# Performance work log

Hardware: AMD Instinct MI355X
Metric: run time of the kernel (lower is better)

The kernel has to match this reference:

```python
import math
import jax, jax.numpy as jnp
import numpy as np

B, L, NS = 8, 1024, 512
D, NH, DN = 512, 8, 256
E, K, HE = 8, 2, 2048
EPS = 1e-5


def setup_inputs() -> dict:
    key = jax.random.key(0)
    ks = jax.random.split(key, 40)
    def rn(i, shape, s=0.02):
        return jax.random.normal(ks[i], shape, jnp.float32) * s
    inp = {
        'x': jax.random.normal(ks[0], (B, L, D), jnp.float32),
        'scene_tokens': jax.random.normal(ks[1], (B, NS, D), jnp.float32),
        't': jax.random.uniform(ks[2], (B,), jnp.float32) * 1000.0,
        # scene LayerNorm (affine)
        'scene_norm_g': jnp.ones((D,), jnp.float32),
        'scene_norm_b': jnp.zeros((D,), jnp.float32),
        # scene cross-attn projections (stored [in,out])
        'ca_wq': rn(3, (D, D)), 'ca_bq': jnp.zeros((D,)),
        'ca_wk': rn(4, (D, D)), 'ca_bk': jnp.zeros((D,)),
        'ca_wv': rn(5, (D, D)), 'ca_bv': jnp.zeros((D,)),
        'ca_wo': rn(6, (D, D)), 'ca_bo': jnp.zeros((D,)),
        # self-attn projections
        'sa_wq': rn(7, (D, D)), 'sa_bq': jnp.zeros((D,)),
        'sa_wk': rn(8, (D, D)), 'sa_bk': jnp.zeros((D,)),
        'sa_wv': rn(9, (D, D)), 'sa_bv': jnp.zeros((D,)),
        'sa_wo': rn(10, (D, D)), 'sa_bo': jnp.zeros((D,)),
        # noise_embed MLP: Linear(D,DN) -> SiLU -> Linear(DN,DN)
        'ne_w1': rn(11, (D, DN)), 'ne_b1': jnp.zeros((DN,)),
        'ne_w2': rn(12, (DN, DN)), 'ne_b2': jnp.zeros((DN,)),
        # AdaLN modulations: Linear(DN, 2D)
        'ncsa_mod_w': rn(13, (DN, 2 * D)), 'ncsa_mod_b': jnp.zeros((2 * D,)),
        'moe_mod_w': rn(14, (DN, 2 * D)), 'moe_mod_b': jnp.zeros((2 * D,)),
        # router
        'router_w': rn(15, (DN, E), s=0.1),
        # stacked pose-branch experts: fc_in D->2*HE, fc_out HE->D
        'fc_in_w': rn(16, (E, D, 2 * HE)), 'fc_in_b': jnp.zeros((E, 2 * HE)),
        'fc_out_w': rn(17, (E, HE, D)), 'fc_out_b': jnp.zeros((E, D)),
    }
    return inp


def _ln(x):
    mu = x.mean(-1, keepdims=True)
    var = ((x - mu) ** 2).mean(-1, keepdims=True)
    return (x - mu) * jax.lax.rsqrt(var + EPS)


def _mha(q_in, k_in, v_in, wq, bq, wk, bk, wv, bv, wo, bo):
    b, lq, d = q_in.shape
    lk = k_in.shape[1]
    hd = d // NH
    q = (q_in @ wq + bq).reshape(b, lq, NH, hd)
    k = (k_in @ wk + bk).reshape(b, lk, NH, hd)
    v = (v_in @ wv + bv).reshape(b, lk, NH, hd)
    att = jnp.einsum('bqhd,bkhd->bhqk', q, k) / math.sqrt(hd)
    p = jax.nn.softmax(att, axis=-1)
    o = jnp.einsum('bhqk,bkhd->bqhd', p, v).reshape(b, lq, d)
    return o @ wo + bo


def reference(x, scene_tokens, t,
              scene_norm_g, scene_norm_b,
              ca_wq, ca_bq, ca_wk, ca_bk, ca_wv, ca_bv, ca_wo, ca_bo,
              sa_wq, sa_bq, sa_wk, sa_bk, sa_wv, sa_bv, sa_wo, sa_bo,
              ne_w1, ne_b1, ne_w2, ne_b2,
              ncsa_mod_w, ncsa_mod_b, moe_mod_w, moe_mod_b,
              router_w, fc_in_w, fc_in_b, fc_out_w, fc_out_b):
    # --- noise clock embedding: sinusoidal(t, D) -> MLP ---
    half = D // 2
    freqs = jnp.exp(-math.log(10000.0) * jnp.arange(half, dtype=jnp.float32) / (half - 1))
    ang = t[:, None] * freqs[None, :]
    temb = jnp.concatenate([jnp.cos(ang), jnp.sin(ang)], axis=-1)  # [B, D]
    nc = jax.nn.silu(temb @ ne_w1 + ne_b1) @ ne_w2 + ne_b2  # [B, DN]

    # --- scene cross-attention ---
    x_in = _ln(x) * scene_norm_g + scene_norm_b
    x = x + _mha(x_in, scene_tokens, scene_tokens,
                 ca_wq, ca_bq, ca_wk, ca_bk, ca_wv, ca_bv, ca_wo, ca_bo)

    # --- noise-conditioned self-attention (AdaLN) ---
    mod = nc @ ncsa_mod_w + ncsa_mod_b
    shift, scale = jnp.split(mod, 2, axis=-1)
    x_ncsa = _ln(x) * (1.0 + scale[:, None, :]) + shift[:, None, :]
    x = x + _mha(x_ncsa, x_ncsa, x_ncsa,
                 sa_wq, sa_bq, sa_wk, sa_bk, sa_wv, sa_bv, sa_wo, sa_bo)

    # --- pose branch: AdaLN + noise-conditioned MoE ---
    mod = nc @ moe_mod_w + moe_mod_b
    shift, scale = jnp.split(mod, 2, axis=-1)
    x_moe = _ln(x) * (1.0 + scale[:, None, :]) + shift[:, None, :]

    logits = nc @ router_w  # temperature = 1.0
    probs = jax.nn.softmax(logits, axis=-1)
    tw, ti = jax.lax.top_k(probs, K)  # [B,K]
    tw = tw / jnp.clip(tw.sum(-1, keepdims=True), 1e-8)

    # gather per-sample selected expert weights -> grouped GEMM
    Wi = fc_in_w[ti]   # [B,K,D,2HE]
    bi = fc_in_b[ti]   # [B,K,2HE]
    h = jnp.einsum('bld,bkdh->bklh', x_moe, Wi) + bi[:, :, None, :]
    val, gate = jnp.split(h, 2, axis=-1)
    hid = val * jax.nn.silu(gate)   # [B,K,L,HE]
    Wo = fc_out_w[ti]  # [B,K,HE,D]
    bo = fc_out_b[ti]  # [B,K,D]
    eo = jnp.einsum('bklh,bkhd->bkld', hid, Wo) + bo[:, :, None, :]
    mixed = jnp.einsum('bk,bkld->bld', tw, eo)

    return x + mixed
```

## Files before the change

### kernel.cpp

```cpp
#include <hip/hip_runtime.h>
#include <math.h>

typedef unsigned short ushort_t;
typedef __attribute__((ext_vector_type(8))) short short8;
typedef __attribute__((ext_vector_type(4))) float f32x4;

#define B_   8
#define L_   1024
#define NS_  512
#define D_   512
#define NH_  8
#define HE_  2048
#define EPS_ 1e-5f

#define MFMA16(a, b, c) __builtin_amdgcn_mfma_f32_16x16x32_bf16(a, b, c, 0, 0, 0)
#define GL2LDS(g, l) __builtin_amdgcn_global_load_lds( \
    (const __attribute__((address_space(1))) unsigned int*)(g), \
    (__attribute__((address_space(3))) unsigned int*)(l), 16, 0, 0)

__device__ __forceinline__ ushort_t f2bf(float f) {
  unsigned u = __float_as_uint(f);
  unsigned r = (u + 0x7fffu + ((u >> 16) & 1u)) >> 16;
  return (ushort_t)r;
}

__device__ __forceinline__ void stage_tile(const ushort_t* __restrict__ g0,
                                           int ld, ushort_t* lds) {
  const int t = threadIdx.x;
  const int w = t >> 6, lane = t & 63;
#pragma unroll
  for (int j = 0; j < 2; ++j) {
    const int c = w * 64 + j * 256 + lane;
    const int row = c >> 2, col = (c & 3) * 8;
    GL2LDS(g0 + (size_t)row * ld + col, lds + (size_t)(w * 64 + j * 256) * 8);
  }
}

__global__ __launch_bounds__(256) void noise_embed(
    const float* __restrict__ t_in,
    const float* __restrict__ w1, const float* __restrict__ b1,
    const float* __restrict__ w2, const float* __restrict__ b2,
    const float* __restrict__ rw,
    float* __restrict__ nc_out,
    float* __restrict__ tw_out, int* __restrict__ ti_out)
{
  const int b = blockIdx.x;
  const int t = threadIdx.x;
  __shared__ float temb[512];
  __shared__ float h1[256];
  __shared__ float ncs[256];
  const float tv = t_in[b];
  {
    float fr = __expf(-logf(10000.0f) * (float)t / 255.0f);
    float ang = tv * fr;
    temb[t] = cosf(ang);
    temb[256 + t] = sinf(ang);
  }
  __syncthreads();
  {
    float s = b1[t];
#pragma unroll 8
    for (int i = 0; i < 512; ++i) s += temb[i] * w1[i * 256 + t];
    h1[t] = s / (1.0f + __expf(-s));
  }
  __syncthreads();
  {
    float s = b2[t];
#pragma unroll 8
    for (int i = 0; i < 256; ++i) s += h1[i] * w2[i * 256 + t];
    ncs[t] = s;
    nc_out[b * 256 + t] = s;
  }
  __syncthreads();
  if (t == 0) {
    float lg[8];
    for (int e = 0; e < 8; ++e) {
      float s = 0.f;
      for (int i = 0; i < 256; ++i) s += ncs[i] * rw[i * 8 + e];
      lg[e] = s;
    }
    float mx = lg[0];
    for (int e = 1; e < 8; ++e) mx = fmaxf(mx, lg[e]);
    float z = 0.f, p[8];
    for (int e = 0; e < 8; ++e) { p[e] = __expf(lg[e] - mx); z += p[e]; }
    for (int e = 0; e < 8; ++e) p[e] /= z;
    int i0 = 0;
    for (int e = 1; e < 8; ++e) if (p[e] > p[i0]) i0 = e;
    int i1 = (i0 == 0) ? 1 : 0;
    for (int e = 0; e < 8; ++e) if (e != i0 && p[e] > p[i1]) i1 = e;
    float s01 = fmaxf(p[i0] + p[i1], 1e-8f);
    tw_out[b * 2 + 0] = p[i0] / s01;
    tw_out[b * 2 + 1] = p[i1] / s01;
    ti_out[b * 2 + 0] = i0;
    ti_out[b * 2 + 1] = i1;
  }
}

__global__ __launch_bounds__(256) void mod_proj(
    const float* __restrict__ nc,
    const float* __restrict__ ncsa_w, const float* __restrict__ ncsa_b,
    const float* __restrict__ moe_w, const float* __restrict__ moe_b,
    float* __restrict__ ncsa_mod, float* __restrict__ moe_mod)
{
  const int b = blockIdx.x, cg = blockIdx.y;
  const int t = threadIdx.x;
  __shared__ float ncs[256];
  ncs[t] = nc[b * 256 + t];
  __syncthreads();
  const int col = cg * 128 + (t & 127);
  const int half = t >> 7;
  const float* wsel = half ? moe_w : ncsa_w;
  const float* bsel = half ? moe_b : ncsa_b;
  float* osel = half ? moe_mod : ncsa_mod;
  float s = bsel[col];
#pragma unroll 8
  for (int i = 0; i < 256; ++i) s += ncs[i] * wsel[(size_t)i * 1024 + col];
  osel[b * 1024 + col] = s;
}

__global__ __launch_bounds__(256) void ln_mod_kernel(
    const float* __restrict__ X, const float* __restrict__ gvec,
    const float* __restrict__ bvec, const float* __restrict__ mod,
    ushort_t* __restrict__ Y)
{
  const int row = blockIdx.x;
  const int b = row >> 10;
  const int t = threadIdx.x;
  const float* xr = X + (size_t)row * 512;
  float2 v = *(const float2*)(xr + t * 2);
  float s = v.x + v.y;
  float q = v.x * v.x + v.y * v.y;
#pragma unroll
  for (int off = 32; off > 0; off >>= 1) {
    s += __shfl_down(s, off, 64);
    q += __shfl_down(q, off, 64);
  }
  __shared__ float ws_[4], wq_[4], smu[1], sinv[1];
  if ((t & 63) == 0) { ws_[t >> 6] = s; wq_[t >> 6] = q; }
  __syncthreads();
  if (t == 0) {
    float S = ws_[0] + ws_[1] + ws_[2] + ws_[3];
    float Q = wq_[0] + wq_[1] + wq_[2] + wq_[3];
    float mu = S * (1.0f / 512.0f);
    float var = Q * (1.0f / 512.0f) - mu * mu;
    smu[0] = mu;
    sinv[0] = rsqrtf(var + EPS_);
  }
  __syncthreads();
  const float mu = smu[0], inv = sinv[0];
  const int d0 = t * 2;
  float scx, scy, shx, shy;
  if (mod) {
    const float* mrow = mod + (size_t)b * 1024;
    scx = 1.0f + mrow[512 + d0]; scy = 1.0f + mrow[512 + d0 + 1];
    shx = mrow[d0];              shy = mrow[d0 + 1];
  } else {
    scx = gvec[d0]; scy = gvec[d0 + 1];
    shx = bvec[d0]; shy = bvec[d0 + 1];
  }
  float ox = (v.x - mu) * inv * scx + shx;
  float oy = (v.y - mu) * inv * scy + shy;
  unsigned pk = (unsigned)f2bf(ox) | ((unsigned)f2bf(oy) << 16);
  *(unsigned*)(Y + (size_t)row * 512 + d0) = pk;
}

__global__ __launch_bounds__(256) void transpose_cvt(
    const float* __restrict__ in, ushort_t* __restrict__ out,
    int R, int C, long ibs, long obs)
{
  __shared__ float tile[32][33];
  const float* src = in + (size_t)blockIdx.z * ibs;
  ushort_t* dst = out + (size_t)blockIdx.z * obs;
  const int c0 = blockIdx.x * 32, r0 = blockIdx.y * 32;
  const int tx = threadIdx.x & 31, ty = threadIdx.x >> 5;
  for (int rr = ty; rr < 32; rr += 8)
    tile[rr][tx] = src[(size_t)(r0 + rr) * C + c0 + tx];
  __syncthreads();
  for (int rr = ty; rr < 32; rr += 8)
    dst[(size_t)(c0 + rr) * R + r0 + tx] = f2bf(tile[tx][rr]);
}

struct P8 { const float* p[8]; };
__global__ __launch_bounds__(256) void transpose_cvt8(
    P8 srcs, ushort_t* __restrict__ out)
{
  __shared__ float tile[32][33];
  const float* src = srcs.p[blockIdx.z];
  ushort_t* dst = out + (size_t)blockIdx.z * 512 * 512;
  const int c0 = blockIdx.x * 32, r0 = blockIdx.y * 32;
  const int tx = threadIdx.x & 31, ty = threadIdx.x >> 5;
  for (int rr = ty; rr < 32; rr += 8)
    tile[rr][tx] = src[(size_t)(r0 + rr) * 512 + c0 + tx];
  __syncthreads();
  for (int rr = ty; rr < 32; rr += 8)
    dst[(size_t)(c0 + rr) * 512 + r0 + tx] = f2bf(tile[tx][rr]);
}

__global__ __launch_bounds__(256) void cvt_bf16(
    const float* __restrict__ in, ushort_t* __restrict__ out)
{
  const int i = (blockIdx.x * 256 + threadIdx.x) * 4;
  float4 v = *(const float4*)(in + i);
  uint2 pk;
  pk.x = (unsigned)f2bf(v.x) | ((unsigned)f2bf(v.y) << 16);
  pk.y = (unsigned)f2bf(v.z) | ((unsigned)f2bf(v.w) << 16);
  *(uint2*)(out + i) = pk;
}

__global__ __launch_bounds__(256) void gemm_bf16(
    const ushort_t* __restrict__ A, const ushort_t* __restrict__ Bt,
    const float* __restrict__ bias, const float* __restrict__ resid,
    void* __restrict__ Cout, int M, int N, int K, int bf16_out)
{
  __shared__ ushort_t As[2][4096];
  __shared__ ushort_t Bs[2][4096];
  const int t = threadIdx.x;
  const int w = t >> 6, lane = t & 63;
  const int quad = lane >> 4, r = lane & 15;
  const int wm = w >> 1, wn = w & 1;
  const int bm = blockIdx.y * 128, bn = blockIdx.x * 128;
  f32x4 acc[4][4];
#pragma unroll
  for (int i = 0; i < 4; ++i)
#pragma unroll
    for (int j = 0; j < 4; ++j) acc[i][j] = (f32x4){0.f, 0.f, 0.f, 0.f};
  const ushort_t* Ab = A + (size_t)bm * K;
  const ushort_t* Bb = Bt + (size_t)bn * K;
  const int NIT = K >> 5;
  stage_tile(Ab, K, As[0]);
  stage_tile(Bb, K, Bs[0]);
  __syncthreads();
  for (int it = 0; it < NIT; ++it) {
    const int cur = it & 1;
    if (it + 1 < NIT) {
      stage_tile(Ab + (it + 1) * 32, K, As[cur ^ 1]);
      stage_tile(Bb + (it + 1) * 32, K, Bs[cur ^ 1]);
    }
    short8 af[4], bfg[4];
#pragma unroll
    for (int i = 0; i < 4; ++i)
      af[i] = *(const short8*)&As[cur][(wm * 64 + i * 16 + r) * 32 + quad * 8];
#pragma unroll
    for (int j = 0; j < 4; ++j)
      bfg[j] = *(const short8*)&Bs[cur][(wn * 64 + j * 16 + r) * 32 + quad * 8];
#pragma unroll
    for (int i = 0; i < 4; ++i)
#pragma unroll
      for (int j = 0; j < 4; ++j)
        acc[i][j] = MFMA16(af[i], bfg[j], acc[i][j]);
    __syncthreads();
  }
  if (bf16_out) {
    ushort_t* Cb = (ushort_t*)Cout;
#pragma unroll
    for (int j = 0; j < 4; ++j) {
      const int col = bn + wn * 64 + j * 16 + r;
      const float bia = bias[col];
#pragma unroll
      for (int i = 0; i < 4; ++i)
#pragma unroll
        for (int reg = 0; reg < 4; ++reg) {
          const int row = bm + wm * 64 + i * 16 + quad * 4 + reg;
          Cb[(size_t)row * N + col] = f2bf(acc[i][j][reg] + bia);
        }
    }
  } else {
    float* Cf = (float*)Cout;
#pragma unroll
    for (int j = 0; j < 4; ++j) {
      const int col = bn + wn * 64 + j * 16 + r;
      const float bia = bias[col];
#pragma unroll
      for (int i = 0; i < 4; ++i)
#pragma unroll
        for (int reg = 0; reg < 4; ++reg) {
          const int row = bm + wm * 64 + i * 16 + quad * 4 + reg;
          float v = acc[i][j][reg] + bia;
          if (resid) v += resid[(size_t)row * N + col];
          Cf[(size_t)row * N + col] = v;
        }
    }
  }
}

__global__ __launch_bounds__(256, 2) void fattn_mfma(
    const ushort_t* __restrict__ Q, const ushort_t* __restrict__ Kmat,
    const ushort_t* __restrict__ V, ushort_t* __restrict__ O, int Lk)
{
  __shared__ __align__(16) ushort_t Ks[64][72];
  __shared__ __align__(16) ushort_t Vt[64][72];
  __shared__ __align__(16) ushort_t Pt[4][32][72];
  const int t = threadIdx.x;
  const int w = t >> 6, lane = t & 63;
  const int quad = lane >> 4, r = lane & 15;
  const int h = blockIdx.y, b = blockIdx.z;
  const int q0 = blockIdx.x * 128;
  const size_t hoff = (size_t)h * 64;
  const ushort_t* Qb = Q + ((size_t)b * 1024 + q0) * 512 + hoff;
  const ushort_t* Kb = Kmat + (size_t)b * Lk * 512 + hoff;
  const ushort_t* Vb = V + (size_t)b * Lk * 512 + hoff;

  short8 qb[2][2];
#pragma unroll
  for (int ct = 0; ct < 2; ++ct)
#pragma unroll
    for (int ki = 0; ki < 2; ++ki)
      qb[ct][ki] = *(const short8*)(Qb + (size_t)(w * 32 + ct * 16 + r) * 512 +
                                    ki * 32 + quad * 8);

  f32x4 oacc[4][2];
#pragma unroll
  for (int rt = 0; rt < 4; ++rt)
#pragma unroll
    for (int ct = 0; ct < 2; ++ct) oacc[rt][ct] = (f32x4){0.f, 0.f, 0.f, 0.f};
  float m_[2] = {-1e30f, -1e30f};
  float l_[2] = {0.f, 0.f};

  uint4 kr[2], vr[2], kn[2], vn[2];
  auto ldkv = [&](int k0, uint4* kp, uint4* vp) {
#pragma unroll
    for (int j = 0; j < 2; ++j) {
      const int dof = (w + 4 * j) * 8;
      kp[j] = *(const uint4*)(Kb + (size_t)(k0 + lane) * 512 + dof);
      vp[j] = *(const uint4*)(Vb + (size_t)(k0 + lane) * 512 + dof);
    }
  };
  auto stkv = [&](const uint4* kp, const uint4* vp) {
#pragma unroll
    for (int j = 0; j < 2; ++j) {
      const int dof = (w + 4 * j) * 8;
      *(uint4*)&Ks[lane][dof] = kp[j];
      const ushort_t* vv = (const ushort_t*)&vp[j];
#pragma unroll
      for (int i = 0; i < 8; ++i) Vt[dof + i][lane] = vv[i];
    }
  };

  ldkv(0, kr, vr);
  const int nch = Lk >> 6;
  for (int c = 0; c < nch; ++c) {
    stkv(kr, vr);
    __syncthreads();
    if (c + 1 < nch) ldkv((c + 1) << 6, kn, vn);

    f32x4 sacc[4][2];
#pragma unroll
    for (int rt = 0; rt < 4; ++rt)
#pragma unroll
      for (int ct = 0; ct < 2; ++ct) sacc[rt][ct] = (f32x4){0.f, 0.f, 0.f, 0.f};
#pragma unroll
    for (int ki = 0; ki < 2; ++ki) {
      short8 kf[4];
#pragma unroll
      for (int rt = 0; rt < 4; ++rt)
        kf[rt] = *(const short8*)&Ks[rt * 16 + r][ki * 32 + quad * 8];
#pragma unroll
      for (int rt = 0; rt < 4; ++rt)
#pragma unroll
        for (int ct = 0; ct < 2; ++ct)
          sacc[rt][ct] = MFMA16(kf[rt], qb[ct][ki], sacc[rt][ct]);
    }

#pragma unroll
    for (int ct = 0; ct < 2; ++ct) {
      float vmax = sacc[0][ct][0];
#pragma unroll
      for (int rt = 0; rt < 4; ++rt)
#pragma unroll
        for (int reg = 0; reg < 4; ++reg) vmax = fmaxf(vmax, sacc[rt][ct][reg]);
      vmax = fmaxf(vmax, __shfl_xor(vmax, 16, 64));
      vmax = fmaxf(vmax, __shfl_xor(vmax, 32, 64));
      const float mnew = fmaxf(m_[ct], vmax * 0.125f);
      const float corr = __expf(m_[ct] - mnew);
      m_[ct] = mnew;
      float ps = 0.f;
#pragma unroll
      for (int rt = 0; rt < 4; ++rt) {
        float p0 = __expf(fmaf(sacc[rt][ct][0], 0.125f, -mnew));
        float p1 = __expf(fmaf(sacc[rt][ct][1], 0.125f, -mnew));
        float p2 = __expf(fmaf(sacc[rt][ct][2], 0.125f, -mnew));
        float p3 = __expf(fmaf(sacc[rt][ct][3], 0.125f, -mnew));
        ps += (p0 + p1) + (p2 + p3);
        uint2 pk;
        pk.x = (unsigned)f2bf(p0) | ((unsigned)f2bf(p1) << 16);
        pk.y = (unsigned)f2bf(p2) | ((unsigned)f2bf(p3) << 16);
        *(uint2*)&Pt[w][ct * 16 + r][rt * 16 + quad * 4] = pk;
      }
      ps += __shfl_xor(ps, 16, 64);
      ps += __shfl_xor(ps, 32, 64);
      l_[ct] = l_[ct] * corr + ps;
#pragma unroll
      for (int rt = 0; rt < 4; ++rt)
#pragma unroll
        for (int reg = 0; reg < 4; ++reg) oacc[rt][ct][reg] *= corr;
    }

#pragma unroll
    for (int ki = 0; ki < 2; ++ki) {
      short8 vf[4], pf[2];
#pragma unroll
      for (int rt = 0; rt < 4; ++rt)
        vf[rt] = *(const short8*)&Vt[rt * 16 + r][ki * 32 + quad * 8];
#pragma unroll
      for (int ct = 0; ct < 2; ++ct)
        pf[ct] = *(const short8*)&Pt[w][ct * 16 + r][ki * 32 + quad * 8];
#pragma unroll
      for (int rt = 0; rt < 4; ++rt)
#pragma unroll
        for (int ct = 0; ct < 2; ++ct)
          oacc[rt][ct] = MFMA16(vf[rt], pf[ct], oacc[rt][ct]);
    }
    __syncthreads();
#pragma unroll
    for (int j = 0; j < 2; ++j) { kr[j] = kn[j]; vr[j] = vn[j]; }
  }

#pragma unroll
  for (int ct = 0; ct < 2; ++ct) {
    const float inv = 1.0f / l_[ct];
    const int qg = q0 + w * 32 + ct * 16 + r;
    ushort_t* op = O + ((size_t)b * 1024 + qg) * 512 + hoff;
#pragma unroll
    for (int rt = 0; rt < 4; ++rt) {
      uint2 pk;
      pk.x = (unsigned)f2bf(oacc[rt][ct][0] * inv) |
             ((unsigned)f2bf(oacc[rt][ct][1] * inv) << 16);
      pk.y = (unsigned)f2bf(oacc[rt][ct][2] * inv) |
             ((unsigned)f2bf(oacc[rt][ct][3] * inv) << 16);
      *(uint2*)(op + rt * 16 + quad * 4) = pk;
    }
  }
}

__global__ __launch_bounds__(256) void moe_fcin(
    const ushort_t* __restrict__ Xm, const ushort_t* __restrict__ WiT,
    const float* __restrict__ Bi, const float* __restrict__ tw,
    const int* __restrict__ ti, ushort_t* __restrict__ Hid, int ks)
{
  __shared__ ushort_t As[2][4096];
  __shared__ ushort_t Bv[2][4096];
  __shared__ ushort_t Bg[2][4096];
  const int t = threadIdx.x;
  const int w = t >> 6, lane = t & 63;
  const int quad = lane >> 4, r = lane & 15;
  const int wm = w >> 1, wn = w & 1;
  const int b = blockIdx.z;
  const int e = ti[b * 2 + ks];
  const float wq = tw[b * 2 + ks];
  const int r0 = blockIdx.y * 128, n0 = blockIdx.x * 128;
  const ushort_t* Ab = Xm + ((size_t)b * 1024 + r0) * 512;
  const ushort_t* Wv = WiT + (size_t)e * 4096 * 512 + (size_t)n0 * 512;
  const ushort_t* Wg = Wv + (size_t)2048 * 512;
  f32x4 av[4][4], ag[4][4];
#pragma unroll
  for (int i = 0; i < 4; ++i)
#pragma unroll
    for (int j = 0; j < 4; ++j) {
      av[i][j] = (f32x4){0.f, 0.f, 0.f, 0.f};
      ag[i][j] = (f32x4){0.f, 0.f, 0.f, 0.f};
    }
  stage_tile(Ab, 512, As[0]);
  stage_tile(Wv, 512, Bv[0]);
  stage_tile(Wg, 512, Bg[0]);
  __syncthreads();
  for (int it = 0; it < 16; ++it) {
    const int cur = it & 1;
    if (it + 1 < 16) {
      stage_tile(Ab + (it + 1) * 32, 512, As[cur ^ 1]);
      stage_tile(Wv + (it + 1) * 32, 512, Bv[cur ^ 1]);
      stage_tile(Wg + (it + 1) * 32, 512, Bg[cur ^ 1]);
    }
    short8 af[4], bv[4], bg[4];
#pragma unroll
    for (int i = 0; i < 4; ++i)
      af[i] = *(const short8*)&As[cur][(wm * 64 + i * 16 + r) * 32 + quad * 8];
#pragma unroll
    for (int j = 0; j < 4; ++j) {
      bv[j] = *(const short8*)&Bv[cur][(wn * 64 + j * 16 + r) * 32 + quad * 8];
      bg[j] = *(const short8*)&Bg[cur][(wn * 64 + j * 16 + r) * 32 + quad * 8];
    }
#pragma unroll
    for (int i = 0; i < 4; ++i)
#pragma unroll
      for (int j = 0; j < 4; ++j) {
        av[i][j] = MFMA16(af[i], bv[j], av[i][j]);
        ag[i][j] = MFMA16(af[i], bg[j], ag[i][j]);
      }
    __syncthreads();
  }
  ushort_t* Hb = Hid + (size_t)b * 1024 * 2048;
#pragma unroll
  for (int j = 0; j < 4; ++j) {
    const int col = n0 + wn * 64 + j * 16 + r;
    const float bval = Bi[(size_t)e * 4096 + col];
    const float bgat = Bi[(size_t)e * 4096 + 2048 + col];
#pragma unroll
    for (int i = 0; i < 4; ++i)
#pragma unroll
      for (int reg = 0; reg < 4; ++reg) {
        const int lrow = r0 + wm * 64 + i * 16 + quad * 4 + reg;
        float vv = av[i][j][reg] + bval;
        float gg = ag[i][j][reg] + bgat;
        float hv = vv * (gg / (1.0f + __expf(-gg))) * wq;
        Hb[(size_t)lrow * 2048 + col] = f2bf(hv);
      }
  }
}

__global__ __launch_bounds__(256) void moe_fcout(
    const ushort_t* __restrict__ Hid, const ushort_t* __restrict__ WoT,
    const float* __restrict__ Bo, const float* __restrict__ X2,
    const float* __restrict__ tw, const int* __restrict__ ti,
    float* __restrict__ Out, int ks, int first)
{
  __shared__ ushort_t As[2][4096];
  __shared__ ushort_t Bs[2][4096];
  const int t = threadIdx.x;
  const int w = t >> 6, lane = t & 63;
  const int quad = lane >> 4, r = lane & 15;
  const int wm = w >> 1, wn = w & 1;
  const int b = blockIdx.z;
  const int e = ti[b * 2 + ks];
  const int r0 = blockIdx.y * 128, n0 = blockIdx.x * 128;
  f32x4 acc[4][4];
#pragma unroll
  for (int i = 0; i < 4; ++i)
#pragma unroll
    for (int j = 0; j < 4; ++j) acc[i][j] = (f32x4){0.f, 0.f, 0.f, 0.f};
  const ushort_t* Ab = Hid + ((size_t)b * 1024 + r0) * 2048;
  const ushort_t* Bb = WoT + (size_t)e * 512 * 2048 + (size_t)n0 * 2048;
  stage_tile(Ab, 2048, As[0]);
  stage_tile(Bb, 2048, Bs[0]);
  __syncthreads();
  for (int it = 0; it < 64; ++it) {
    const int cur = it & 1;
    if (it + 1 < 64) {
      stage_tile(Ab + (it + 1) * 32, 2048, As[cur ^ 1]);
      stage_tile(Bb + (it + 1) * 32, 2048, Bs[cur ^ 1]);
    }
    short8 af[4], bfg[4];
#pragma unroll
    for (int i = 0; i < 4; ++i)
      af[i] = *(const short8*)&As[cur][(wm * 64 + i * 16 + r) * 32 + quad * 8];
#pragma unroll
    for (int j = 0; j < 4; ++j)
      bfg[j] = *(const short8*)&Bs[cur][(wn * 64 + j * 16 + r) * 32 + quad * 8];
#pragma unroll
    for (int i = 0; i < 4; ++i)
#pragma unroll
      for (int j = 0; j < 4; ++j)
        acc[i][j] = MFMA16(af[i], bfg[j], acc[i][j]);
    __syncthreads();
  }
  const int e0 = ti[b * 2], e1 = ti[b * 2 + 1];
  const float tw0 = tw[b * 2], tw1 = tw[b * 2 + 1];
#pragma unroll
  for (int j = 0; j < 4; ++j) {
    const int col = n0 + wn * 64 + j * 16 + r;
    const float badd = first ? (tw0 * Bo[(size_t)e0 * 512 + col] +
                                tw1 * Bo[(size_t)e1 * 512 + col]) : 0.f;
#pragma unroll
    for (int i = 0; i < 4; ++i)
#pragma unroll
      for (int reg = 0; reg < 4; ++reg) {
        const size_t row = (size_t)b * 1024 + r0 + wm * 64 + i * 16 + quad * 4 + reg;
        const size_t idx = row * 512 + col;
        const float base = first ? X2[idx] : Out[idx];
        Out[idx] = base + acc[i][j][reg] + badd;
      }
  }
}

extern "C" void kernel_launch(void* const* d_in, const int* in_sizes, int n_in,
                              void* d_out, int out_size, void* d_ws, size_t ws_size,
                              hipStream_t stream) {
  const float* x        = (const float*)d_in[0];
  const float* scene    = (const float*)d_in[1];
  const float* t_in     = (const float*)d_in[2];
  const float* sn_g     = (const float*)d_in[3];
  const float* sn_b     = (const float*)d_in[4];
  const float* ca_wq    = (const float*)d_in[5];
  const float* ca_bq    = (const float*)d_in[6];
  const float* ca_wk    = (const float*)d_in[7];
  const float* ca_bk    = (const float*)d_in[8];
  const float* ca_wv    = (const float*)d_in[9];
  const float* ca_bv    = (const float*)d_in[10];
  const float* ca_wo    = (const float*)d_in[11];
  const float* ca_bo    = (const float*)d_in[12];
  const float* sa_wq    = (const float*)d_in[13];
  const float* sa_bq    = (const float*)d_in[14];
  const float* sa_wk    = (const float*)d_in[15];
  const float* sa_bk    = (const float*)d_in[16];
  const float* sa_wv    = (const float*)d_in[17];
  const float* sa_bv    = (const float*)d_in[18];
  const float* sa_wo    = (const float*)d_in[19];
  const float* sa_bo    = (const float*)d_in[20];
  const float* ne_w1    = (const float*)d_in[21];
  const float* ne_b1    = (const float*)d_in[22];
  const float* ne_w2    = (const float*)d_in[23];
  const float* ne_b2    = (const float*)d_in[24];
  const float* ncsa_w   = (const float*)d_in[25];
  const float* ncsa_b   = (const float*)d_in[26];
  const float* moe_w    = (const float*)d_in[27];
  const float* moe_b    = (const float*)d_in[28];
  const float* router_w = (const float*)d_in[29];
  const float* fc_in_w  = (const float*)d_in[30];
  const float* fc_in_b  = (const float*)d_in[31];
  const float* fc_out_w = (const float*)d_in[32];
  const float* fc_out_b = (const float*)d_in[33];
  float* out = (float*)d_out;

  char* W = (char*)d_ws;
  const size_t MB = 1u << 20;
  float* ncsa_mod = (float*)W;
  float* moe_mod  = ncsa_mod + 8192;
  float* tw       = moe_mod + 8192;
  int*   ti       = (int*)(tw + 16);
  float* nc_ws    = (float*)(ti + 16);
  ushort_t* wT      = (ushort_t*)(W + 1 * MB);
  ushort_t* fciT    = (ushort_t*)(W + 5 * MB);
  ushort_t* fcoT    = (ushort_t*)(W + 37 * MB);
  ushort_t* xin_bf  = (ushort_t*)(W + 53 * MB);
  ushort_t* attn_bf = xin_bf;
  ushort_t* scene_bf= (ushort_t*)(W + 61 * MB);
  ushort_t* qf = (ushort_t*)(W + 65 * MB);
  ushort_t* kf = (ushort_t*)(W + 73 * MB);
  ushort_t* vf = (ushort_t*)(W + 81 * MB);
  ushort_t* hid = (ushort_t*)(W + 61 * MB);
  float* x1 = out;

  const int WSZ = 512 * 512;

  noise_embed<<<dim3(B_), dim3(256), 0, stream>>>(
      t_in, ne_w1, ne_b1, ne_w2, ne_b2, router_w, nc_ws, tw, ti);
  mod_proj<<<dim3(B_, 8), dim3(256), 0, stream>>>(
      nc_ws, ncsa_w, ncsa_b, moe_w, moe_b, ncsa_mod, moe_mod);

  P8 dsrc;
  dsrc.p[0] = ca_wq; dsrc.p[1] = ca_wk; dsrc.p[2] = ca_wv; dsrc.p[3] = ca_wo;
  dsrc.p[4] = sa_wq; dsrc.p[5] = sa_wk; dsrc.p[6] = sa_wv; dsrc.p[7] = sa_wo;
  transpose_cvt8<<<dim3(16, 16, 8), 256, 0, stream>>>(dsrc, wT);
  transpose_cvt<<<dim3(128, 16, 8), 256, 0, stream>>>(fc_in_w, fciT, 512, 4096,
                                                      (long)512 * 4096, (long)512 * 4096);
  transpose_cvt<<<dim3(16, 64, 8), 256, 0, stream>>>(fc_out_w, fcoT, 2048, 512,
                                                     (long)2048 * 512, (long)2048 * 512);
  cvt_bf16<<<dim3(2048), 256, 0, stream>>>(scene, scene_bf);

  ln_mod_kernel<<<dim3(8192), 256, 0, stream>>>(x, sn_g, sn_b, nullptr, xin_bf);
  gemm_bf16<<<dim3(4, 64), 256, 0, stream>>>(xin_bf, wT + 0 * WSZ, ca_bq, nullptr, qf, 8192, 512, 512, 1);
  gemm_bf16<<<dim3(4, 32), 256, 0, stream>>>(scene_bf, wT + 1 * WSZ, ca_bk, nullptr, kf, 4096, 512, 512, 1);
  gemm_bf16<<<dim3(4, 32), 256, 0, stream>>>(scene_bf, wT + 2 * WSZ, ca_bv, nullptr, vf, 4096, 512, 512, 1);
  fattn_mfma<<<dim3(8, NH_, B_), 256, 0, stream>>>(qf, kf, vf, attn_bf, NS_);
  gemm_bf16<<<dim3(4, 64), 256, 0, stream>>>(attn_bf, wT + 3 * WSZ, ca_bo, x, x1, 8192, 512, 512, 0);

  ln_mod_kernel<<<dim3(8192), 256, 0, stream>>>(x1, nullptr, nullptr, ncsa_mod, xin_bf);
  gemm_bf16<<<dim3(4, 64), 256, 0, stream>>>(xin_bf, wT + 4 * WSZ, sa_bq, nullptr, qf, 8192, 512, 512, 1);
  gemm_bf16<<<dim3(4, 64), 256, 0, stream>>>(xin_bf, wT + 5 * WSZ, sa_bk, nullptr, kf, 8192, 512, 512, 1);
  gemm_bf16<<<dim3(4, 64), 256, 0, stream>>>(xin_bf, wT + 6 * WSZ, sa_bv, nullptr, vf, 8192, 512, 512, 1);
  fattn_mfma<<<dim3(8, NH_, B_), 256, 0, stream>>>(qf, kf, vf, attn_bf, L_);
  gemm_bf16<<<dim3(4, 64), 256, 0, stream>>>(attn_bf, wT + 7 * WSZ, sa_bo, out, out, 8192, 512, 512, 0);

  ln_mod_kernel<<<dim3(8192), 256, 0, stream>>>(out, nullptr, nullptr, moe_mod, xin_bf);
  moe_fcin<<<dim3(16, 8, B_), 256, 0, stream>>>(xin_bf, fciT, fc_in_b, tw, ti, hid, 0);
  moe_fcout<<<dim3(4, 8, B_), 256, 0, stream>>>(hid, fcoT, fc_out_b, out, tw, ti, out, 0, 1);
  moe_fcin<<<dim3(16, 8, B_), 256, 0, stream>>>(xin_bf, fciT, fc_in_b, tw, ti, hid, 1);
  moe_fcout<<<dim3(4, 8, B_), 256, 0, stream>>>(hid, fcoT, fc_out_b, out, tw, ti, out, 1, 0);
}
```

Before: 832.8 us.

## Shrink attention query tile, remap blocks per XCD, and parallelize noise embedding

The flash-attention kernel now handles 64 queries per block instead of 128, which doubles the grid to 1024 one-dimensional blocks. Block indices are remapped so that blocks sharing a batch and head land on the same XCD for K/V cache reuse. Occupancy is raised to 4 blocks per CU, and MFMA sections are bracketed with s_setprio. The noise-embedding kernel moves to 1024 threads, splitting each dot product four ways with shuffle reductions and running the router logits in parallel. The trade-off is that each K/V tile staged in LDS is reused by fewer queries, so K/V traffic rises.

```diff
diff --git a/kernel.cpp b/kernel.cpp
--- a/kernel.cpp
+++ b/kernel.cpp
@@ -36,7 +36,7 @@
   }
 }
 
-__global__ __launch_bounds__(256) void noise_embed(
+__global__ __launch_bounds__(1024) void noise_embed(
     const float* __restrict__ t_in,
     const float* __restrict__ w1, const float* __restrict__ b1,
     const float* __restrict__ w2, const float* __restrict__ b2,
@@ -49,36 +49,57 @@
   __shared__ float temb[512];
   __shared__ float h1[256];
   __shared__ float ncs[256];
+  __shared__ float lg[8];
   const float tv = t_in[b];
+  if (t < 512) {
+    const int k = t & 255;
+    float fr = __expf(-logf(10000.0f) * (float)k / 255.0f);
+    float ang = tv * fr;
+    temb[t] = (t < 256) ? cosf(ang) : sinf(ang);
+  }
+  __syncthreads();
+  const int col = t >> 2, part = t & 3;
   {
-    float fr = __expf(-logf(10000.0f) * (float)t / 255.0f);
-    float ang = tv * fr;
-    temb[t] = cosf(ang);
-    temb[256 + t] = sinf(ang);
+    float s = 0.f;
+    const float* wp = w1 + (size_t)(part * 128) * 256 + col;
+    const float* tp = temb + part * 128;
+#pragma unroll 32
+    for (int i = 0; i < 128; ++i) s += tp[i] * wp[(size_t)i * 256];
+    s += __shfl_xor(s, 1, 64);
+    s += __shfl_xor(s, 2, 64);
+    if (part == 0) {
+      s += b1[col];
+      h1[col] = s / (1.0f + __expf(-s));
+    }
   }
   __syncthreads();
   {
-    float s = b1[t];
-#pragma unroll 8
-    for (int i = 0; i < 512; ++i) s += temb[i] * w1[i * 256 + t];
-    h1[t] = s / (1.0f + __expf(-s));
-  }
-  __syncthreads();
-  {
-    float s = b2[t];
-#pragma unroll 8
-    for (int i = 0; i < 256; ++i) s += h1[i] * w2[i * 256 + t];
-    ncs[t] = s;
-    nc_out[b * 256 + t] = s;
+    float s = 0.f;
+    const float* wp = w2 + (size_t)(part * 64) * 256 + col;
+    const float* hp = h1 + part * 64;
+#pragma unroll 32
+    for (int i = 0; i < 64; ++i) s += hp[i] * wp[(size_t)i * 256];
+    s += __shfl_xor(s, 1, 64);
+    s += __shfl_xor(s, 2, 64);
+    if (part == 0) {
+      s += b2[col];
+      ncs[col] = s;
+      nc_out[b * 256 + col] = s;
+    }
+  }
+  __syncthreads();
+  if (t < 64) {
+    const int e = t >> 3, seg = t & 7;
+    float s = 0.f;
+#pragma unroll
+    for (int i = 0; i < 32; ++i) s += ncs[seg * 32 + i] * rw[(seg * 32 + i) * 8 + e];
+    s += __shfl_xor(s, 1, 64);
+    s += __shfl_xor(s, 2, 64);
+    s += __shfl_xor(s, 4, 64);
+    if (seg == 0) lg[e] = s;
   }
   __syncthreads();
   if (t == 0) {
-    float lg[8];
-    for (int e = 0; e < 8; ++e) {
-      float s = 0.f;
-      for (int i = 0; i < 256; ++i) s += ncs[i] * rw[i * 8 + e];
-      lg[e] = s;
-    }
     float mx = lg[0];
     for (int e = 1; e < 8; ++e) mx = fmaxf(mx, lg[e]);
     float z = 0.f, p[8];
@@ -113,7 +134,7 @@
   const float* bsel = half ? moe_b : ncsa_b;
   float* osel = half ? moe_mod : ncsa_mod;
   float s = bsel[col];
-#pragma unroll 8
+#pragma unroll 16
   for (int i = 0; i < 256; ++i) s += ncs[i] * wsel[(size_t)i * 1024 + col];
   osel[b * 1024 + col] = s;
 }
@@ -283,38 +304,38 @@
   }
 }
 
-__global__ __launch_bounds__(256, 2) void fattn_mfma(
+__global__ __launch_bounds__(256, 4) void fattn_mfma(
     const ushort_t* __restrict__ Q, const ushort_t* __restrict__ Kmat,
     const ushort_t* __restrict__ V, ushort_t* __restrict__ O, int Lk)
 {
   __shared__ __align__(16) ushort_t Ks[64][72];
   __shared__ __align__(16) ushort_t Vt[64][72];
-  __shared__ __align__(16) ushort_t Pt[4][32][72];
+  __shared__ __align__(16) ushort_t Pt[4][16][72];
   const int t = threadIdx.x;
   const int w = t >> 6, lane = t & 63;
   const int quad = lane >> 4, r = lane & 15;
-  const int h = blockIdx.y, b = blockIdx.z;
-  const int q0 = blockIdx.x * 128;
+  const int bid = blockIdx.x;
+  const int xcd = bid & 7, jj = bid >> 3;
+  const int g = xcd + 8 * (jj >> 4);
+  const int qi = jj & 15;
+  const int h = g & 7, b = g >> 3;
+  const int q0 = qi * 64;
   const size_t hoff = (size_t)h * 64;
   const ushort_t* Qb = Q + ((size_t)b * 1024 + q0) * 512 + hoff;
   const ushort_t* Kb = Kmat + (size_t)b * Lk * 512 + hoff;
   const ushort_t* Vb = V + (size_t)b * Lk * 512 + hoff;
 
-  short8 qb[2][2];
-#pragma unroll
-  for (int ct = 0; ct < 2; ++ct)
-#pragma unroll
-    for (int ki = 0; ki < 2; ++ki)
-      qb[ct][ki] = *(const short8*)(Qb + (size_t)(w * 32 + ct * 16 + r) * 512 +
-                                    ki * 32 + quad * 8);
-
-  f32x4 oacc[4][2];
-#pragma unroll
-  for (int rt = 0; rt < 4; ++rt)
-#pragma unroll
-    for (int ct = 0; ct < 2; ++ct) oacc[rt][ct] = (f32x4){0.f, 0.f, 0.f, 0.f};
-  float m_[2] = {-1e30f, -1e30f};
-  float l_[2] = {0.f, 0.f};
+  short8 qb[2];
+#pragma unroll
+  for (int ki = 0; ki < 2; ++ki)
+    qb[ki] = *(const short8*)(Qb + (size_t)(w * 16 + r) * 512 +
+                              ki * 32 + quad * 8);
+
+  f32x4 oacc[4];
+#pragma unroll
+  for (int rt = 0; rt < 4; ++rt) oacc[rt] = (f32x4){0.f, 0.f, 0.f, 0.f};
+  float m_ = -1e30f;
+  float l_ = 0.f;
 
   uint4 kr[2], vr[2], kn[2], vn[2];
   auto ldkv = [&](int k0, uint4* kp, uint4* vp) {
@@ -343,11 +364,10 @@
     __syncthreads();
     if (c + 1 < nch) ldkv((c + 1) << 6, kn, vn);
 
-    f32x4 sacc[4][2];
-#pragma unroll
-    for (int rt = 0; rt < 4; ++rt)
-#pragma unroll
-      for (int ct = 0; ct < 2; ++ct) sacc[rt][ct] = (f32x4){0.f, 0.f, 0.f, 0.f};
+    f32x4 sacc[4];
+#pragma unroll
+    for (int rt = 0; rt < 4; ++rt) sacc[rt] = (f32x4){0.f, 0.f, 0.f, 0.f};
+    __builtin_amdgcn_s_setprio(1);
 #pragma unroll
     for (int ki = 0; ki < 2; ++ki) {
       short8 kf[4];
@@ -356,77 +376,72 @@
         kf[rt] = *(const short8*)&Ks[rt * 16 + r][ki * 32 + quad * 8];
 #pragma unroll
       for (int rt = 0; rt < 4; ++rt)
-#pragma unroll
-        for (int ct = 0; ct < 2; ++ct)
-          sacc[rt][ct] = MFMA16(kf[rt], qb[ct][ki], sacc[rt][ct]);
-    }
-
-#pragma unroll
-    for (int ct = 0; ct < 2; ++ct) {
-      float vmax = sacc[0][ct][0];
+        sacc[rt] = MFMA16(kf[rt], qb[ki], sacc[rt]);
+    }
+    __builtin_amdgcn_s_setprio(0);
+
+    {
+      float vmax = sacc[0][0];
 #pragma unroll
       for (int rt = 0; rt < 4; ++rt)
 #pragma unroll
-        for (int reg = 0; reg < 4; ++reg) vmax = fmaxf(vmax, sacc[rt][ct][reg]);
+        for (int reg = 0; reg < 4; ++reg) vmax = fmaxf(vmax, sacc[rt][reg]);
       vmax = fmaxf(vmax, __shfl_xor(vmax, 16, 64));
       vmax = fmaxf(vmax, __shfl_xor(vmax, 32, 64));
-      const float mnew = fmaxf(m_[ct], vmax * 0.125f);
-      const float corr = __expf(m_[ct] - mnew);
-      m_[ct] = mnew;
+      const float mnew = fmaxf(m_, vmax * 0.125f);
+      const float corr = __expf(m_ - mnew);
+      m_ = mnew;
       float ps = 0.f;
 #pragma unroll
       for (int rt = 0; rt < 4; ++rt) {
-        float p0 = __expf(fmaf(sacc[rt][ct][0], 0.125f, -mnew));
-        float p1 = __expf(fmaf(sacc[rt][ct][1], 0.125f, -mnew));
-        float p2 = __expf(fmaf(sacc[rt][ct][2], 0.125f, -mnew));
-        float p3 = __expf(fmaf(sacc[rt][ct][3], 0.125f, -mnew));
+        float p0 = __expf(fmaf(sacc[rt][0], 0.125f, -mnew));
+        float p1 = __expf(fmaf(sacc[rt][1], 0.125f, -mnew));
+        float p2 = __expf(fmaf(sacc[rt][2], 0.125f, -mnew));
+        float p3 = __expf(fmaf(sacc[rt][3], 0.125f, -mnew));
         ps += (p0 + p1) + (p2 + p3);
         uint2 pk;
         pk.x = (unsigned)f2bf(p0) | ((unsigned)f2bf(p1) << 16);
         pk.y = (unsigned)f2bf(p2) | ((unsigned)f2bf(p3) << 16);
-        *(uint2*)&Pt[w][ct * 16 + r][rt * 16 + quad * 4] = pk;
+        *(uint2*)&Pt[w][r][rt * 16 + quad * 4] = pk;
       }
       ps += __shfl_xor(ps, 16, 64);
       ps += __shfl_xor(ps, 32, 64);
-      l_[ct] = l_[ct] * corr + ps;
+      l_ = l_ * corr + ps;
 #pragma unroll
       for (int rt = 0; rt < 4; ++rt)
 #pragma unroll
-        for (int reg = 0; reg < 4; ++reg) oacc[rt][ct][reg] *= corr;
-    }
-
+        for (int reg = 0; reg < 4; ++reg) oacc[rt][reg] *= corr;
+    }
+
+    __builtin_amdgcn_s_setprio(1);
 #pragma unroll
     for (int ki = 0; ki < 2; ++ki) {
-      short8 vf[4], pf[2];
+      short8 vf[4], pf;
 #pragma unroll
       for (int rt = 0; rt < 4; ++rt)
         vf[rt] = *(const short8*)&Vt[rt * 16 + r][ki * 32 + quad * 8];
-#pragma unroll
-      for (int ct = 0; ct < 2; ++ct)
-        pf[ct] = *(const short8*)&Pt[w][ct * 16 + r][ki * 32 + quad * 8];
+      pf = *(const short8*)&Pt[w][r][ki * 32 + quad * 8];
 #pragma unroll
       for (int rt = 0; rt < 4; ++rt)
-#pragma unroll
-        for (int ct = 0; ct < 2; ++ct)
-          oacc[rt][ct] = MFMA16(vf[rt], pf[ct], oacc[rt][ct]);
-    }
+        oacc[rt] = MFMA16(vf[rt], pf, oacc[rt]);
+    }
+    __builtin_amdgcn_s_setprio(0);
     __syncthreads();
 #pragma unroll
     for (int j = 0; j < 2; ++j) { kr[j] = kn[j]; vr[j] = vn[j]; }
   }
 
-#pragma unroll
-  for (int ct = 0; ct < 2; ++ct) {
-    const float inv = 1.0f / l_[ct];
-    const int qg = q0 + w * 32 + ct * 16 + r;
+  {
+    const float inv = 1.0f / l_;
+    const int qg = q0 + w * 16 + r;
     ushort_t* op = O + ((size_t)b * 1024 + qg) * 512 + hoff;
 #pragma unroll
     for (int rt = 0; rt < 4; ++rt) {
       uint2 pk;
-      pk.x = (unsigned)f2bf(oacc[rt][ct][0] * inv) |
-             ((unsigned)f2bf(oacc[rt][ct][1] * inv) << 16);
-      pk.y = (unsigned)f2bf(oacc[rt][ct][2] * inv) |
-             ((unsigned)f2bf(oacc[rt][ct][3] * inv) << 16);
+      pk.x = (unsigned)f2bf(oacc[rt][0] * inv) |
+             ((unsigned)f2bf(oacc[rt][1] * inv) << 16);
+      pk.y = (unsigned)f2bf(oacc[rt][2] * inv) |
+             ((unsigned)f2bf(oacc[rt][3] * inv) << 16);
       *(uint2*)(op + rt * 16 + quad * 4) = pk;
     }
   }
@@ -631,7 +646,7 @@
 
   const int WSZ = 512 * 512;
 
-  noise_embed<<<dim3(B_), dim3(256), 0, stream>>>(
+  noise_embed<<<dim3(B_), dim3(1024), 0, stream>>>(
       t_in, ne_w1, ne_b1, ne_w2, ne_b2, router_w, nc_ws, tw, ti);
   mod_proj<<<dim3(B_, 8), dim3(256), 0, stream>>>(
       nc_ws, ncsa_w, ncsa_b, moe_w, moe_b, ncsa_mod, moe_mod);
@@ -650,14 +665,14 @@
   gemm_bf16<<<dim3(4, 64), 256, 0, stream>>>(xin_bf, wT + 0 * WSZ, ca_bq, nullptr, qf, 8192, 512, 512, 1);
   gemm_bf16<<<dim3(4, 32), 256, 0, stream>>>(scene_bf, wT + 1 * WSZ, ca_bk, nullptr, kf, 4096, 512, 512, 1);
   gemm_bf16<<<dim3(4, 32), 256, 0, stream>>>(scene_bf, wT + 2 * WSZ, ca_bv, nullptr, vf, 4096, 512, 512, 1);
-  fattn_mfma<<<dim3(8, NH_, B_), 256, 0, stream>>>(qf, kf, vf, attn_bf, NS_);
+  fattn_mfma<<<dim3(1024), 256, 0, stream>>>(qf, kf, vf, attn_bf, NS_);
   gemm_bf16<<<dim3(4, 64), 256, 0, stream>>>(attn_bf, wT + 3 * WSZ, ca_bo, x, x1, 8192, 512, 512, 0);
 
   ln_mod_kernel<<<dim3(8192), 256, 0, stream>>>(x1, nullptr, nullptr, ncsa_mod, xin_bf);
   gemm_bf16<<<dim3(4, 64), 256, 0, stream>>>(xin_bf, wT + 4 * WSZ, sa_bq, nullptr, qf, 8192, 512, 512, 1);
   gemm_bf16<<<dim3(4, 64), 256, 0, stream>>>(xin_bf, wT + 5 * WSZ, sa_bk, nullptr, kf, 8192, 512, 512, 1);
   gemm_bf16<<<dim3(4, 64), 256, 0, stream>>>(xin_bf, wT + 6 * WSZ, sa_bv, nullptr, vf, 8192, 512, 512, 1);
-  fattn_mfma<<<dim3(8, NH_, B_), 256, 0, stream>>>(qf, kf, vf, attn_bf, L_);
+  fattn_mfma<<<dim3(1024), 256, 0, stream>>>(qf, kf, vf, attn_bf, L_);
   gemm_bf16<<<dim3(4, 64), 256, 0, stream>>>(attn_bf, wT + 7 * WSZ, sa_bo, out, out, 8192, 512, 512, 0);
 
   ln_mod_kernel<<<dim3(8192), 256, 0, stream>>>(out, nullptr, nullptr, moe_mod, xin_bf);
```

Measured after the change: 831.7 us. About the same (-0.1%).
